# Kernel tuning notes

Measured on AMD Instinct MI355X. Metric: run time of the kernel, lower is better.

The kernel has to match this reference:

```python
import jax, jax.numpy as jnp
import numpy as np
from jax import lax

D_MODEL = 768
N_LAYER = 4
D_STATE = 16
D_CONV = 4
EXPAND = 2
VOCAB = 32000
B = 1
L = 1024
D_INNER = D_MODEL * EXPAND
EPS = 1e-5


def setup_inputs() -> dict:
    key = jax.random.key(0)
    ks = jax.random.split(key, 8)
    s = 0.02
    A_row = jnp.log(jnp.arange(1, D_STATE + 1, dtype=jnp.float32))  # log(1..N)
    return {
        "idx": jax.random.randint(ks[0], (B, L), 0, VOCAB),
        "embed": jax.random.normal(ks[1], (VOCAB, D_MODEL), jnp.float32) * s,
        "norm_w": jnp.ones((N_LAYER, D_MODEL), jnp.float32),
        "W_in": jax.random.normal(ks[2], (N_LAYER, 2 * D_INNER, D_MODEL), jnp.float32) * s,
        "conv_w": jax.random.normal(ks[3], (N_LAYER, D_INNER, 1, D_CONV), jnp.float32) * s,
        "conv_b": jnp.zeros((N_LAYER, D_INNER), jnp.float32),
        "W_x": jax.random.normal(ks[4], (N_LAYER, 2 * D_STATE + 1, D_INNER), jnp.float32) * s,
        "dt_w": jax.random.normal(ks[5], (N_LAYER, D_INNER, 1), jnp.float32) * s,
        "dt_b": jnp.zeros((N_LAYER, D_INNER), jnp.float32),
        "A_log": jnp.tile(A_row, (N_LAYER, D_INNER, 1)),
        "Dp": jnp.ones((N_LAYER, D_INNER), jnp.float32),
        "out_w": jax.random.normal(ks[6], (N_LAYER, D_MODEL, D_INNER), jnp.float32) * s,
        "norm_f_w": jnp.ones((D_MODEL,), jnp.float32),
    }


def rmsnorm(x, w):
    return x / jnp.sqrt(jnp.mean(x * x, axis=-1, keepdims=True) + EPS) * w


def selective_scan(xc, W_x, dt_w, dt_b, A_log, Dp):
    # xc: [B, L, D_INNER]
    A = -jnp.exp(A_log)                               # [D, N]
    xp = xc @ W_x.T                                   # [B, L, 2N+1]
    dt_r = xp[..., :1]
    Bv = xp[..., 1:1 + D_STATE]                       # [B, L, N]
    Cv = xp[..., 1 + D_STATE:]                        # [B, L, N]
    dt = jax.nn.softplus(dt_r * dt_w[:, 0] + dt_b)    # [B, L, D]
    dA = jnp.exp(dt[..., None] * A)                   # [B, L, D, N]
    dBx = dt[..., None] * Bv[:, :, None, :] * xc[..., None]  # [B, L, D, N]

    def step(h, inp):
        dA_t, dBx_t, C_t = inp
        h = dA_t * h + dBx_t                          # [B, D, N]
        y = jnp.einsum('bdn,bn->bd', h, C_t)          # [B, D]
        return h, y

    h0 = jnp.zeros((xc.shape[0], D_INNER, D_STATE), xc.dtype)
    _, ys = lax.scan(step, h0, (dA.transpose(1, 0, 2, 3),
                                dBx.transpose(1, 0, 2, 3),
                                Cv.transpose(1, 0, 2)))
    return ys.transpose(1, 0, 2) + xc * Dp            # [B, L, D]


def mamba_block(x, W_in, conv_w, conv_b, W_x, dt_w, dt_b, A_log, Dp, out_w):
    xz = x @ W_in.T                                   # [B, L, 2*D_INNER]
    x_ssm, z = jnp.split(xz, 2, axis=-1)
    # depthwise causal conv1d (torch pads both sides then keeps first L == left pad only)
    xc = lax.conv_general_dilated(x_ssm.transpose(0, 2, 1), conv_w, (1,),
                                  [(D_CONV - 1, 0)],
                                  feature_group_count=D_INNER,
                                  dimension_numbers=('NCH', 'OIH', 'NCH'))
    xc = (xc + conv_b[None, :, None]).transpose(0, 2, 1)
    xc = jax.nn.silu(xc)
    y = selective_scan(xc, W_x, dt_w, dt_b, A_log, Dp)
    y = y * jax.nn.silu(z)
    return y @ out_w.T


def reference(idx, embed, norm_w, W_in, conv_w, conv_b, W_x, dt_w, dt_b, A_log, Dp, out_w, norm_f_w):
    x = embed[idx]  # dropout in eval mode == identity
    for i in range(N_LAYER):
        x = x + mamba_block(rmsnorm(x, norm_w[i]), W_in[i], conv_w[i], conv_b[i],
                            W_x[i], dt_w[i], dt_b[i], A_log[i], Dp[i], out_w[i])
    x = rmsnorm(x, norm_f_w)
    logits = x @ embed.T  # tied lm_head
    return logits
```

## Files before the change

### kernel.cpp

```cpp
#include <hip/hip_runtime.h>

#define D_MODEL 768
#define D_INNER 1536
#define D_XZ    3072
#define D_STATE 16
#define LSEQ    1024
#define NCHUNK  32
#define CLEN    32

typedef float  floatx4 __attribute__((ext_vector_type(4)));
typedef __bf16 bf16x2  __attribute__((ext_vector_type(2)));
typedef __bf16 bf16x8  __attribute__((ext_vector_type(8)));

__device__ __forceinline__ float softplus_f(float x) {
  float e = __expf(-fabsf(x));
  return fmaxf(x, 0.f) + __logf(1.f + e);
}
__device__ __forceinline__ float silu_f(float x) {
  return x / (1.f + __expf(-x));
}
__device__ __forceinline__ void gload_lds16(const void* g, void* l) {
  __builtin_amdgcn_global_load_lds(
      (const __attribute__((address_space(1))) void*)g,
      (__attribute__((address_space(3))) void*)l, 16, 0, 0);
}

__global__ __launch_bounds__(256) void k_cvt(const float* __restrict__ src,
                                             __bf16* __restrict__ dst) {
  size_t i = ((size_t)blockIdx.x * 256 + threadIdx.x) * 8;
  float4 a = *(const float4*)(src + i);
  float4 b = *(const float4*)(src + i + 4);
  bf16x8 o;
  o[0] = (__bf16)a.x; o[1] = (__bf16)a.y; o[2] = (__bf16)a.z; o[3] = (__bf16)a.w;
  o[4] = (__bf16)b.x; o[5] = (__bf16)b.y; o[6] = (__bf16)b.z; o[7] = (__bf16)b.w;
  *(bf16x8*)(dst + i) = o;
}

__global__ __launch_bounds__(256) void k_gather(const float* __restrict__ embed,
                                                const int* __restrict__ idx,
                                                float* __restrict__ x) {
  int t = blockIdx.x;
  int tok = idx[t];
  const float* src = embed + (size_t)tok * D_MODEL;
  float* dst = x + (size_t)t * D_MODEL;
  for (int c = threadIdx.x; c < D_MODEL; c += 256) dst[c] = src[c];
}

__global__ __launch_bounds__(256) void k_rmsnorm_bf(const float* __restrict__ x,
                                                    const float* __restrict__ w,
                                                    __bf16* __restrict__ o) {
  int lane = threadIdx.x & 63;
  int row = blockIdx.x * 4 + (threadIdx.x >> 6);
  const float* xr = x + (size_t)row * D_MODEL;
  float2 v[6];
  float ss = 0.f;
#pragma unroll
  for (int i = 0; i < 6; i++) {
    v[i] = *(const float2*)(xr + lane * 2 + i * 128);
    ss += v[i].x * v[i].x + v[i].y * v[i].y;
  }
#pragma unroll
  for (int m = 32; m; m >>= 1) ss += __shfl_xor(ss, m, 64);
  float r = rsqrtf(ss * (1.f / 768.f) + 1e-5f);
  __bf16* orow = o + (size_t)row * D_MODEL;
#pragma unroll
  for (int i = 0; i < 6; i++) {
    float2 wv = *(const float2*)(w + lane * 2 + i * 128);
    bf16x2 p;
    p[0] = (__bf16)(v[i].x * r * wv.x);
    p[1] = (__bf16)(v[i].y * r * wv.y);
    *(bf16x2*)(orow + lane * 2 + i * 128) = p;
  }
}

template <int TM>
__global__ __launch_bounds__(256) void k_gemm_bb(const __bf16* __restrict__ A,
                                                 const __bf16* __restrict__ B,
                                                 const float* res, float* __restrict__ C,
                                                 int M, int N, int K, int mTiles) {
  constexpr int MT = TM / 32;
  __shared__ __attribute__((aligned(16))) __bf16 As[TM * 32];
  __shared__ __attribute__((aligned(16))) __bf16 Bs[128 * 32];
  const int tid = threadIdx.x;
  const int lane = tid & 63, wave = tid >> 6;
  const int fr = lane & 15, q = lane >> 4, kq = q * 8;

  int id = blockIdx.x;
  int per = gridDim.x >> 3;
  int v = (id & 7) * per + (id >> 3);
  int nt = v / mTiles, mt_ = v % mTiles;
  const int Mblk = mt_ * TM, Nblk = nt * 128;

  const int wm = (wave & 1) * (TM / 2), wn = (wave >> 1) * 64;

  const int row_s = tid >> 2;
  const int col_s = (tid & 3) * 8;
  const __bf16* Ag = A + (size_t)(Mblk + row_s) * K + col_s;
  const __bf16* Bg = B + (size_t)(Nblk + row_s) * K + col_s;
  __bf16* Asd = &As[tid * 8];
  __bf16* Bsd = &Bs[tid * 8];

  floatx4 acc[MT][4];
#pragma unroll
  for (int i = 0; i < MT; i++)
#pragma unroll
    for (int j = 0; j < 4; j++) {
      floatx4 z = {0.f, 0.f, 0.f, 0.f};
      acc[i][j] = z;
    }

  for (int k0 = 0; k0 < K; k0 += 32) {
    __syncthreads();
#pragma unroll
    for (int i = 0; i < TM / 64; i++)
      gload_lds16(Ag + (size_t)(64 * i) * K + k0, Asd + i * 2048);
#pragma unroll
    for (int i = 0; i < 2; i++)
      gload_lds16(Bg + (size_t)(64 * i) * K + k0, Bsd + i * 2048);
    __syncthreads();
    bf16x8 af[MT], bfr[4];
#pragma unroll
    for (int mt = 0; mt < MT; mt++) af[mt] = *(const bf16x8*)&As[(wm + mt * 16 + fr) * 32 + kq];
#pragma unroll
    for (int ntl = 0; ntl < 4; ntl++) bfr[ntl] = *(const bf16x8*)&Bs[(wn + ntl * 16 + fr) * 32 + kq];
#pragma unroll
    for (int mt = 0; mt < MT; mt++)
#pragma unroll
      for (int ntl = 0; ntl < 4; ntl++)
        acc[mt][ntl] = __builtin_amdgcn_mfma_f32_16x16x32_bf16(af[mt], bfr[ntl], acc[mt][ntl], 0, 0, 0);
  }

#pragma unroll
  for (int mt = 0; mt < MT; mt++)
#pragma unroll
    for (int ntl = 0; ntl < 4; ntl++) {
      int r = Mblk + wm + mt * 16 + q * 4;
      int c = Nblk + wn + ntl * 16 + fr;
#pragma unroll
      for (int i = 0; i < 4; i++) {
        size_t o = (size_t)(r + i) * N + c;
        float vv = acc[mt][ntl][i];
        if (res) vv += res[o];
        C[o] = vv;
      }
    }
}

__global__ __launch_bounds__(256) void k_xpconv(const float* __restrict__ xz,
                                                const float* __restrict__ cw4,
                                                const float* __restrict__ cb,
                                                const float* __restrict__ Wx,
                                                float* __restrict__ xc,
                                                float* __restrict__ xp) {
  __shared__ float red[4][33];
  int t = blockIdx.x;
  int wave = threadIdx.x >> 6, lane = threadIdx.x & 63;
  float acc[33];
#pragma unroll
  for (int j = 0; j < 33; j++) acc[j] = 0.f;
  for (int ii = 0; ii < 6; ii++) {
    int k = wave * 384 + ii * 64 + lane;
    float4 w = *(const float4*)(cw4 + (size_t)k * 4);
    float wv[4] = {w.x, w.y, w.z, w.w};
    float vv = cb[k];
#pragma unroll
    for (int jj = 0; jj < 4; jj++) {
      int ts = t - 3 + jj;
      if (ts >= 0) vv += wv[jj] * xz[(size_t)ts * D_XZ + k];
    }
    float xcv = silu_f(vv);
    xc[(size_t)t * D_INNER + k] = xcv;
#pragma unroll
    for (int j = 0; j < 33; j++) acc[j] += xcv * Wx[(size_t)j * D_INNER + k];
  }
#pragma unroll
  for (int j = 0; j < 33; j++) {
    float s = acc[j];
#pragma unroll
    for (int m = 32; m; m >>= 1) s += __shfl_xor(s, m, 64);
    if (lane == j) red[wave][j] = s;
  }
  __syncthreads();
  int j = threadIdx.x;
  if (j < 33) xp[(size_t)t * 33 + j] = red[0][j] + red[1][j] + red[2][j] + red[3][j];
}

__global__ __launch_bounds__(256) void k_scan1(const float* __restrict__ xp,
                                               const float* __restrict__ xc,
                                               const float* __restrict__ dtw,
                                               const float* __restrict__ dtb,
                                               const float* __restrict__ Alog,
                                               float* __restrict__ hend,
                                               float* __restrict__ Pp) {
  __shared__ float sxp[CLEN * 33];
  int c = blockIdx.x;
  int d = blockIdx.y * 256 + threadIdx.x;
  for (int i = threadIdx.x; i < CLEN * 33; i += 256) sxp[i] = xp[(size_t)c * CLEN * 33 + i];
  __syncthreads();
  float Av[16];
#pragma unroll
  for (int n = 0; n < 16; n++) Av[n] = -__expf(Alog[(size_t)d * 16 + n]);
  float w_ = dtw[d], b_ = dtb[d];
  float h[16], P[16];
#pragma unroll
  for (int n = 0; n < 16; n++) { h[n] = 0.f; P[n] = 1.f; }
  const float* xcc = xc + (size_t)(c * CLEN) * D_INNER + d;
  for (int tl = 0; tl < CLEN; tl++) {
    float dtr = sxp[tl * 33];
    float xv = xcc[(size_t)tl * D_INNER];
    float dt = softplus_f(dtr * w_ + b_);
    float sx = dt * xv;
#pragma unroll
    for (int n = 0; n < 16; n++) {
      float dA = __expf(dt * Av[n]);
      h[n] = dA * h[n] + sx * sxp[tl * 33 + 1 + n];
      P[n] *= dA;
    }
  }
  size_t o = ((size_t)c * D_INNER + d) * 16;
#pragma unroll
  for (int n = 0; n < 16; n++) { hend[o + n] = h[n]; Pp[o + n] = P[n]; }
}

__global__ __launch_bounds__(256) void k_comb(const float* __restrict__ hend,
                                              const float* __restrict__ Pp,
                                              float* __restrict__ h0) {
  int i = blockIdx.x * 256 + threadIdx.x;
  float h = 0.f;
  for (int c = 0; c < NCHUNK; c++) {
    h0[(size_t)c * (D_INNER * 16) + i] = h;
    h = Pp[(size_t)c * (D_INNER * 16) + i] * h + hend[(size_t)c * (D_INNER * 16) + i];
  }
}

__global__ __launch_bounds__(256) void k_scan2(const float* __restrict__ xp,
                                               const float* __restrict__ xc,
                                               const float* __restrict__ xz,
                                               const float* __restrict__ dtw,
                                               const float* __restrict__ dtb,
                                               const float* __restrict__ Alog,
                                               const float* __restrict__ Dp,
                                               const float* __restrict__ h0,
                                               __bf16* __restrict__ g) {
  __shared__ float sxp[CLEN * 33];
  int c = blockIdx.x;
  int d = blockIdx.y * 256 + threadIdx.x;
  for (int i = threadIdx.x; i < CLEN * 33; i += 256) sxp[i] = xp[(size_t)c * CLEN * 33 + i];
  __syncthreads();
  float Av[16];
#pragma unroll
  for (int n = 0; n < 16; n++) Av[n] = -__expf(Alog[(size_t)d * 16 + n]);
  float w_ = dtw[d], b_ = dtb[d], Dv = Dp[d];
  float h[16];
  size_t ho = ((size_t)c * D_INNER + d) * 16;
#pragma unroll
  for (int n = 0; n < 16; n++) h[n] = h0[ho + n];
  for (int tl = 0; tl < CLEN; tl++) {
    int t = c * CLEN + tl;
    float dtr = sxp[tl * 33];
    float xv = xc[(size_t)t * D_INNER + d];
    float dt = softplus_f(dtr * w_ + b_);
    float sx = dt * xv;
    float y = 0.f;
#pragma unroll
    for (int n = 0; n < 16; n++) {
      float dA = __expf(dt * Av[n]);
      h[n] = dA * h[n] + sx * sxp[tl * 33 + 1 + n];
      y += h[n] * sxp[tl * 33 + 17 + n];
    }
    float z = xz[(size_t)t * D_XZ + D_INNER + d];
    g[(size_t)t * D_INNER + d] = (__bf16)((y + xv * Dv) * silu_f(z));
  }
}

extern "C" void kernel_launch(void* const* d_in, const int* in_sizes, int n_in,
                              void* d_out, int out_size, void* d_ws, size_t ws_size,
                              hipStream_t stream) {
  const int*   idx     = (const int*)d_in[0];
  const float* embed   = (const float*)d_in[1];
  const float* norm_w  = (const float*)d_in[2];
  const float* W_in    = (const float*)d_in[3];
  const float* conv_w  = (const float*)d_in[4];
  const float* conv_b  = (const float*)d_in[5];
  const float* W_x     = (const float*)d_in[6];
  const float* dt_w    = (const float*)d_in[7];
  const float* dt_b    = (const float*)d_in[8];
  const float* A_log   = (const float*)d_in[9];
  const float* Dp      = (const float*)d_in[10];
  const float* out_w   = (const float*)d_in[11];
  const float* norm_fw = (const float*)d_in[12];
  float* out = (float*)d_out;

  float*  x    = (float*)d_ws;
  __bf16* xnb  = (__bf16*)(x + 786432);
  float*  xp   = (float*)(xnb + 786432);
  float*  Pp   = xp + 33792;
  float*  h0b  = Pp + 786432;
  __bf16* gbf  = (__bf16*)(h0b + 786432);
  __bf16* pool = gbf + 1572864;
  __bf16* W_in_bf  = pool;
  __bf16* out_w_bf = pool + 9437184;
  float*  xz   = (float*)(out_w_bf + 4718592);
  float*  xc   = xz + 3145728;
  float*  hend = xc + 1572864;
  __bf16* emb_bf = pool;

  k_cvt<<<4608, 256, 0, stream>>>(W_in, W_in_bf);
  k_cvt<<<2304, 256, 0, stream>>>(out_w, out_w_bf);

  k_gather<<<1024, 256, 0, stream>>>(embed, idx, x);

  for (int l = 0; l < 4; l++) {
    k_rmsnorm_bf<<<256, 256, 0, stream>>>(x, norm_w + (size_t)l * D_MODEL, xnb);
    k_gemm_bb<128><<<192, 256, 0, stream>>>(xnb, W_in_bf + (size_t)l * D_XZ * D_MODEL,
                                            nullptr, xz, 1024, D_XZ, D_MODEL, 8);
    k_xpconv<<<1024, 256, 0, stream>>>(xz, conv_w + (size_t)l * D_INNER * 4,
                                       conv_b + (size_t)l * D_INNER,
                                       W_x + (size_t)l * 33 * D_INNER, xc, xp);
    k_scan1<<<dim3(NCHUNK, 6), 256, 0, stream>>>(xp, xc, dt_w + (size_t)l * D_INNER,
                                                 dt_b + (size_t)l * D_INNER,
                                                 A_log + (size_t)l * D_INNER * 16, hend, Pp);
    k_comb<<<(D_INNER * 16) / 256, 256, 0, stream>>>(hend, Pp, h0b);
    k_scan2<<<dim3(NCHUNK, 6), 256, 0, stream>>>(xp, xc, xz, dt_w + (size_t)l * D_INNER,
                                                 dt_b + (size_t)l * D_INNER,
                                                 A_log + (size_t)l * D_INNER * 16,
                                                 Dp + (size_t)l * D_INNER, h0b, gbf);
    k_gemm_bb<64><<<96, 256, 0, stream>>>(gbf, out_w_bf + (size_t)l * D_MODEL * D_INNER,
                                          x, x, 1024, D_MODEL, D_INNER, 16);
  }

  k_cvt<<<12000, 256, 0, stream>>>(embed, emb_bf);
  k_rmsnorm_bf<<<256, 256, 0, stream>>>(x, norm_fw, xnb);
  k_gemm_bb<128><<<2000, 256, 0, stream>>>(xnb, emb_bf, nullptr, out,
                                           1024, 32000, D_MODEL, 8);
}
```

Measured before the change: 916.4 us.

## Double-buffer GEMM LDS loads, retile small GEMMs, fold chunk combine into scan2

The bf16 MFMA GEMM now double-buffers its LDS tiles. It issues the next K-slice's global_load_lds before computing the current one and waits with explicit vmcnt counts, so global loads overlap MFMA work. The GEMM is also templated on tile N, and the in_proj and out_proj GEMMs use smaller tiles so more blocks are launched on the many CUs. The separate k_comb kernel is removed: each scan2 block recomputes its starting state by serially combining all earlier chunk end-states, trading redundant reads of hend/Pp for one less launch and one less buffer.

```diff
diff --git a/kernel.cpp b/kernel.cpp
--- a/kernel.cpp
+++ b/kernel.cpp
@@ -23,6 +23,14 @@
   __builtin_amdgcn_global_load_lds(
       (const __attribute__((address_space(1))) void*)g,
       (__attribute__((address_space(3))) void*)l, 16, 0, 0);
+}
+
+template <int N> __device__ __forceinline__ void waitcnt_vm() {
+  static_assert(N == 0 || N == 2 || N == 3 || N == 4, "unsupported vmcnt");
+  if constexpr (N == 0) asm volatile("s_waitcnt vmcnt(0)" ::: "memory");
+  else if constexpr (N == 2) asm volatile("s_waitcnt vmcnt(2)" ::: "memory");
+  else if constexpr (N == 3) asm volatile("s_waitcnt vmcnt(3)" ::: "memory");
+  else if constexpr (N == 4) asm volatile("s_waitcnt vmcnt(4)" ::: "memory");
 }
 
 __global__ __launch_bounds__(256) void k_cvt(const float* __restrict__ src,
@@ -73,14 +81,18 @@
   }
 }
 
-template <int TM>
+template <int TM, int TN>
 __global__ __launch_bounds__(256) void k_gemm_bb(const __bf16* __restrict__ A,
                                                  const __bf16* __restrict__ B,
                                                  const float* res, float* __restrict__ C,
                                                  int M, int N, int K, int mTiles) {
-  constexpr int MT = TM / 32;
-  __shared__ __attribute__((aligned(16))) __bf16 As[TM * 32];
-  __shared__ __attribute__((aligned(16))) __bf16 Bs[128 * 32];
+  constexpr int MT  = TM / 32;
+  constexpr int NTL = TN / 32;
+  constexpr int NLA = TM / 64;
+  constexpr int NLB = TN / 64;
+  constexpr int NL  = NLA + NLB;
+  __shared__ __attribute__((aligned(16))) __bf16 As[2][TM * 32];
+  __shared__ __attribute__((aligned(16))) __bf16 Bs[2][TN * 32];
   const int tid = threadIdx.x;
   const int lane = tid & 63, wave = tid >> 6;
   const int fr = lane & 15, q = lane >> 4, kq = q * 8;
@@ -89,51 +101,69 @@
   int per = gridDim.x >> 3;
   int v = (id & 7) * per + (id >> 3);
   int nt = v / mTiles, mt_ = v % mTiles;
-  const int Mblk = mt_ * TM, Nblk = nt * 128;
-
-  const int wm = (wave & 1) * (TM / 2), wn = (wave >> 1) * 64;
+  const int Mblk = mt_ * TM, Nblk = nt * TN;
+
+  const int wm = (wave & 1) * (TM / 2), wn = (wave >> 1) * (TN / 2);
 
   const int row_s = tid >> 2;
   const int col_s = (tid & 3) * 8;
   const __bf16* Ag = A + (size_t)(Mblk + row_s) * K + col_s;
   const __bf16* Bg = B + (size_t)(Nblk + row_s) * K + col_s;
-  __bf16* Asd = &As[tid * 8];
-  __bf16* Bsd = &Bs[tid * 8];
-
-  floatx4 acc[MT][4];
+
+  floatx4 acc[MT][NTL];
 #pragma unroll
   for (int i = 0; i < MT; i++)
 #pragma unroll
-    for (int j = 0; j < 4; j++) {
+    for (int j = 0; j < NTL; j++) {
       floatx4 z = {0.f, 0.f, 0.f, 0.f};
       acc[i][j] = z;
     }
 
-  for (int k0 = 0; k0 < K; k0 += 32) {
-    __syncthreads();
-#pragma unroll
-    for (int i = 0; i < TM / 64; i++)
-      gload_lds16(Ag + (size_t)(64 * i) * K + k0, Asd + i * 2048);
-#pragma unroll
-    for (int i = 0; i < 2; i++)
-      gload_lds16(Bg + (size_t)(64 * i) * K + k0, Bsd + i * 2048);
-    __syncthreads();
-    bf16x8 af[MT], bfr[4];
-#pragma unroll
-    for (int mt = 0; mt < MT; mt++) af[mt] = *(const bf16x8*)&As[(wm + mt * 16 + fr) * 32 + kq];
-#pragma unroll
-    for (int ntl = 0; ntl < 4; ntl++) bfr[ntl] = *(const bf16x8*)&Bs[(wn + ntl * 16 + fr) * 32 + kq];
+  const int KT = K >> 5;
+
+#pragma unroll
+  for (int i = 0; i < NLA; i++)
+    gload_lds16(Ag + (size_t)(64 * i) * K, &As[0][tid * 8 + i * 2048]);
+#pragma unroll
+  for (int i = 0; i < NLB; i++)
+    gload_lds16(Bg + (size_t)(64 * i) * K, &Bs[0][tid * 8 + i * 2048]);
+
+  for (int kt = 0; kt < KT; kt++) {
+    const int cur = kt & 1;
+    if (kt + 1 < KT) {
+      const int k1 = (kt + 1) << 5;
+#pragma unroll
+      for (int i = 0; i < NLA; i++)
+        gload_lds16(Ag + (size_t)(64 * i) * K + k1, &As[cur ^ 1][tid * 8 + i * 2048]);
+#pragma unroll
+      for (int i = 0; i < NLB; i++)
+        gload_lds16(Bg + (size_t)(64 * i) * K + k1, &Bs[cur ^ 1][tid * 8 + i * 2048]);
+      waitcnt_vm<NL>();
+    } else {
+      waitcnt_vm<0>();
+    }
+    __builtin_amdgcn_s_barrier();
+
+    bf16x8 af[MT], bfr[NTL];
 #pragma unroll
     for (int mt = 0; mt < MT; mt++)
-#pragma unroll
-      for (int ntl = 0; ntl < 4; ntl++)
+      af[mt] = *(const bf16x8*)&As[cur][(wm + mt * 16 + fr) * 32 + kq];
+#pragma unroll
+    for (int ntl = 0; ntl < NTL; ntl++)
+      bfr[ntl] = *(const bf16x8*)&Bs[cur][(wn + ntl * 16 + fr) * 32 + kq];
+#pragma unroll
+    for (int mt = 0; mt < MT; mt++)
+#pragma unroll
+      for (int ntl = 0; ntl < NTL; ntl++)
         acc[mt][ntl] = __builtin_amdgcn_mfma_f32_16x16x32_bf16(af[mt], bfr[ntl], acc[mt][ntl], 0, 0, 0);
+
+    __builtin_amdgcn_s_barrier();
   }
 
 #pragma unroll
   for (int mt = 0; mt < MT; mt++)
 #pragma unroll
-    for (int ntl = 0; ntl < 4; ntl++) {
+    for (int ntl = 0; ntl < NTL; ntl++) {
       int r = Mblk + wm + mt * 16 + q * 4;
       int c = Nblk + wn + ntl * 16 + fr;
 #pragma unroll
@@ -222,17 +252,6 @@
   for (int n = 0; n < 16; n++) { hend[o + n] = h[n]; Pp[o + n] = P[n]; }
 }
 
-__global__ __launch_bounds__(256) void k_comb(const float* __restrict__ hend,
-                                              const float* __restrict__ Pp,
-                                              float* __restrict__ h0) {
-  int i = blockIdx.x * 256 + threadIdx.x;
-  float h = 0.f;
-  for (int c = 0; c < NCHUNK; c++) {
-    h0[(size_t)c * (D_INNER * 16) + i] = h;
-    h = Pp[(size_t)c * (D_INNER * 16) + i] * h + hend[(size_t)c * (D_INNER * 16) + i];
-  }
-}
-
 __global__ __launch_bounds__(256) void k_scan2(const float* __restrict__ xp,
                                                const float* __restrict__ xc,
                                                const float* __restrict__ xz,
@@ -240,7 +259,8 @@
                                                const float* __restrict__ dtb,
                                                const float* __restrict__ Alog,
                                                const float* __restrict__ Dp,
-                                               const float* __restrict__ h0,
+                                               const float* __restrict__ hend,
+                                               const float* __restrict__ Pp,
                                                __bf16* __restrict__ g) {
   __shared__ float sxp[CLEN * 33];
   int c = blockIdx.x;
@@ -252,9 +272,20 @@
   for (int n = 0; n < 16; n++) Av[n] = -__expf(Alog[(size_t)d * 16 + n]);
   float w_ = dtw[d], b_ = dtb[d], Dv = Dp[d];
   float h[16];
-  size_t ho = ((size_t)c * D_INNER + d) * 16;
-#pragma unroll
-  for (int n = 0; n < 16; n++) h[n] = h0[ho + n];
+#pragma unroll
+  for (int n = 0; n < 16; n++) h[n] = 0.f;
+  for (int c2 = 0; c2 < c; c2++) {
+    size_t o = ((size_t)c2 * D_INNER + d) * 16;
+#pragma unroll
+    for (int n4 = 0; n4 < 4; n4++) {
+      float4 hv = *(const float4*)(hend + o + n4 * 4);
+      float4 pv = *(const float4*)(Pp + o + n4 * 4);
+      h[n4 * 4 + 0] = pv.x * h[n4 * 4 + 0] + hv.x;
+      h[n4 * 4 + 1] = pv.y * h[n4 * 4 + 1] + hv.y;
+      h[n4 * 4 + 2] = pv.z * h[n4 * 4 + 2] + hv.z;
+      h[n4 * 4 + 3] = pv.w * h[n4 * 4 + 3] + hv.w;
+    }
+  }
   for (int tl = 0; tl < CLEN; tl++) {
     int t = c * CLEN + tl;
     float dtr = sxp[tl * 33];
@@ -295,8 +326,7 @@
   __bf16* xnb  = (__bf16*)(x + 786432);
   float*  xp   = (float*)(xnb + 786432);
   float*  Pp   = xp + 33792;
-  float*  h0b  = Pp + 786432;
-  __bf16* gbf  = (__bf16*)(h0b + 786432);
+  __bf16* gbf  = (__bf16*)(Pp + 786432);
   __bf16* pool = gbf + 1572864;
   __bf16* W_in_bf  = pool;
   __bf16* out_w_bf = pool + 9437184;
@@ -312,25 +342,24 @@
 
   for (int l = 0; l < 4; l++) {
     k_rmsnorm_bf<<<256, 256, 0, stream>>>(x, norm_w + (size_t)l * D_MODEL, xnb);
-    k_gemm_bb<128><<<192, 256, 0, stream>>>(xnb, W_in_bf + (size_t)l * D_XZ * D_MODEL,
-                                            nullptr, xz, 1024, D_XZ, D_MODEL, 8);
+    k_gemm_bb<64, 128><<<384, 256, 0, stream>>>(xnb, W_in_bf + (size_t)l * D_XZ * D_MODEL,
+                                                nullptr, xz, 1024, D_XZ, D_MODEL, 16);
     k_xpconv<<<1024, 256, 0, stream>>>(xz, conv_w + (size_t)l * D_INNER * 4,
                                        conv_b + (size_t)l * D_INNER,
                                        W_x + (size_t)l * 33 * D_INNER, xc, xp);
     k_scan1<<<dim3(NCHUNK, 6), 256, 0, stream>>>(xp, xc, dt_w + (size_t)l * D_INNER,
                                                  dt_b + (size_t)l * D_INNER,
                                                  A_log + (size_t)l * D_INNER * 16, hend, Pp);
-    k_comb<<<(D_INNER * 16) / 256, 256, 0, stream>>>(hend, Pp, h0b);
     k_scan2<<<dim3(NCHUNK, 6), 256, 0, stream>>>(xp, xc, xz, dt_w + (size_t)l * D_INNER,
                                                  dt_b + (size_t)l * D_INNER,
                                                  A_log + (size_t)l * D_INNER * 16,
-                                                 Dp + (size_t)l * D_INNER, h0b, gbf);
-    k_gemm_bb<64><<<96, 256, 0, stream>>>(gbf, out_w_bf + (size_t)l * D_MODEL * D_INNER,
-                                          x, x, 1024, D_MODEL, D_INNER, 16);
+                                                 Dp + (size_t)l * D_INNER, hend, Pp, gbf);
+    k_gemm_bb<64, 64><<<192, 256, 0, stream>>>(gbf, out_w_bf + (size_t)l * D_MODEL * D_INNER,
+                                               x, x, 1024, D_MODEL, D_INNER, 16);
   }
 
   k_cvt<<<12000, 256, 0, stream>>>(embed, emb_bf);
   k_rmsnorm_bf<<<256, 256, 0, stream>>>(x, norm_fw, xnb);
-  k_gemm_bb<128><<<2000, 256, 0, stream>>>(xnb, emb_bf, nullptr, out,
-                                           1024, 32000, D_MODEL, 8);
-}
+  k_gemm_bb<128, 128><<<2000, 256, 0, stream>>>(xnb, emb_bf, nullptr, out,
+                                                1024, 32000, D_MODEL, 8);
+}
```

Result: faster. 865.1 us (-5.6%).
